# Performance work log

Hardware: AMD Instinct MI355X
Metric: run time of the kernel (lower is better)

## Reference

```python
import jax, jax.numpy as jnp
import numpy as np

C, H, W = 8, 2048, 2048
NUM_SEG = 64      # labels 0..63; label 0 = background (ndimage.label convention)
SIGMA_AGG = 0.5


def setup_inputs() -> dict:
    key = jax.random.key(0)
    k1, k2, k3 = jax.random.split(key, 3)
    pred_similarities = jax.random.normal(k1, (C, H, W), dtype=jnp.float32)
    kernel_labels = jax.random.randint(k2, (H, W), 0, NUM_SEG).astype(jnp.int32)
    region_labels = jax.random.randint(k3, (H, W), 0, NUM_SEG).astype(jnp.int32)
    # masks are 1 exactly where a connected component exists (labels > 0),
    # matching what ndimage.label would produce from these masks
    kernels_mask = (kernel_labels > 0).astype(jnp.float32)
    regions_mask = (region_labels > 0).astype(jnp.float32)
    return {
        "pred_similarities": pred_similarities,
        "regions_mask": regions_mask,
        "kernels_mask": kernels_mask,
        "kernel_labels": kernel_labels,
        "region_labels": region_labels,
    }


def reference(pred_similarities, regions_mask, kernels_mask, kernel_labels, region_labels):
    h, w = kernel_labels.shape
    kl = kernel_labels.reshape(-1)  # [N]
    rl = region_labels.reshape(-1)  # [N]

    # per-label cardinality, broadcast back to pixels (label 0 contributes 0
    # because the mask is 0 there, matching the original's untouched zeros)
    kcard = jax.ops.segment_sum(kernels_mask.reshape(-1), kl, num_segments=NUM_SEG)[kl].reshape(h, w)
    rcard = jax.ops.segment_sum(regions_mask.reshape(-1), rl, num_segments=NUM_SEG)[rl].reshape(h, w)

    # per-channel, per-kernel-component sum of pred, broadcast back per pixel
    c = pred_similarities.shape[0]
    pred_flat = pred_similarities.reshape(c, -1)  # [C, N]
    seg = jax.vmap(lambda p: jax.ops.segment_sum(p, kl, num_segments=NUM_SEG))(pred_flat)  # [C, NUM_SEG]
    Gk = jnp.where(kl[None, :] > 0, seg[:, kl], 0.0).reshape(c, h, w)
    Gk = Gk / (kcard + 1.0)[None]

    Fp = pred_similarities * regions_mask[None]
    diff = Fp - Gk
    # torch.linalg.norm over the whole tensor -> scalar Frobenius norm
    D = jnp.maximum(jnp.sqrt(jnp.sum(diff * diff)) - SIGMA_AGG, 0.0)
    per_pixel = jnp.log(D * D + 1.0) / (rcard + 1.0)  # [H, W]

    num_region = jnp.maximum(jnp.max(region_labels), 1).astype(per_pixel.dtype)
    return jnp.sum(per_pixel) / num_region
```

## Files before the change

kernel.cpp:

```cpp
#include <hip/hip_runtime.h>
#include <math.h>

#define NPIX (2048*2048)
#define NGROUPS (NPIX/32)
#define NBLOCKS 1024
#define NWAVES (NBLOCKS*4)

#define WS_FLOATS 3072
#define LROW 17
#define LTAB (64*LROW)
#define LDS_FLOATS (3*LTAB)

typedef __attribute__((ext_vector_type(8))) short short8;
typedef __attribute__((ext_vector_type(4))) float f32x4;
typedef __attribute__((ext_vector_type(2))) unsigned short u16x2;
typedef __attribute__((ext_vector_type(4))) unsigned int u32x4;

__device__ inline unsigned int pk_trunc_bf16(float lo, float hi) {
    return __builtin_amdgcn_perm(__float_as_uint(hi), __float_as_uint(lo), 0x07060302u);
}
__device__ inline unsigned int pk_lab(int lo, int hi) {
    return __builtin_amdgcn_perm((unsigned)hi, (unsigned)lo, 0x05040100u);
}
__device__ inline unsigned int onehot_pair(unsigned int x) {
    u16x2 xv = __builtin_bit_cast(u16x2, x);
    u16x2 y  = __builtin_elementwise_min(xv, (u16x2){1, 1});
    u16x2 w  = y - (u16x2){1, 1};
    return __builtin_bit_cast(unsigned int, w) & 0x3F803F80u;
}

__global__ __launch_bounds__(256, 4) void agg_mfma(
    const float* __restrict__ pred,
    const int*   __restrict__ kl,
    const int*   __restrict__ rl,
    float* __restrict__ ws)
{
    const int tid  = threadIdx.x;
    const int wv   = tid >> 6;
    const int lane = tid & 63;
    const int quad = lane >> 4;
    const int col  = lane & 15;
    const int c8   = col & 7;
    const bool lowcol = (col < 8);
    const unsigned int cpack   = (unsigned)col * 0x00010001u;
    const unsigned int hiconst = (col == 8) ? 0x3F803F80u : 0u;

    f32x4 acc[12];
    #pragma unroll
    for (int s = 0; s < 12; ++s) acc[s] = (f32x4){0.f, 0.f, 0.f, 0.f};

    const float* predc = pred + (size_t)c8 * NPIX;
    const int gw = blockIdx.x * 4 + wv;

    for (int g = gw; g < NGROUPS; g += NWAVES) {
        const int p8 = g * 32 + quad * 8;

        const int4 ka = *(const int4*)(kl + p8);
        const int4 kb = *(const int4*)(kl + p8 + 4);
        const int4 ra = *(const int4*)(rl + p8);
        const int4 rb = *(const int4*)(rl + p8 + 4);
        const float4 pa = *(const float4*)(predc + p8);
        const float4 pb = *(const float4*)(predc + p8 + 4);

        const int   klv[8] = {ka.x, ka.y, ka.z, ka.w, kb.x, kb.y, kb.z, kb.w};
        const int   rlv[8] = {ra.x, ra.y, ra.z, ra.w, rb.x, rb.y, rb.z, rb.w};
        const float pv[8]  = {pa.x, pa.y, pa.z, pa.w, pb.x, pb.y, pb.z, pb.w};

        float pr[8];
        #pragma unroll
        for (int j = 0; j < 8; ++j) pr[j] = (rlv[j] > 0) ? pv[j] : 0.f;

        unsigned int b1p[4], b2p[4], kp[4], rp[4];
        #pragma unroll
        for (int i = 0; i < 4; ++i) {
            const int j0 = 2 * i, j1 = 2 * i + 1;
            const float a0 = lowcol ? pv[j0] : pr[j0];
            const float a1 = lowcol ? pv[j1] : pr[j1];
            b1p[i] = pk_trunc_bf16(a0, a1);
            const unsigned int q = pk_trunc_bf16(pr[j0] * pr[j0], pr[j1] * pr[j1]);
            b2p[i] = lowcol ? q : hiconst;
            kp[i] = pk_lab(klv[j0], klv[j1]);
            rp[i] = pk_lab(rlv[j0], rlv[j1]);
        }
        const short8 b1 = __builtin_bit_cast(short8, (u32x4){b1p[0], b1p[1], b1p[2], b1p[3]});
        const short8 b2 = __builtin_bit_cast(short8, (u32x4){b2p[0], b2p[1], b2p[2], b2p[3]});

        #pragma unroll
        for (int t = 0; t < 4; ++t) {
            const unsigned int tp = cpack + (unsigned)t * 0x00100010u;
            u32x4 ohk, ohr;
            #pragma unroll
            for (int i = 0; i < 4; ++i) {
                ohk[i] = onehot_pair(kp[i] ^ tp);
                ohr[i] = onehot_pair(rp[i] ^ tp);
            }
            const short8 ak = __builtin_bit_cast(short8, ohk);
            const short8 ar = __builtin_bit_cast(short8, ohr);
            acc[t]     = __builtin_amdgcn_mfma_f32_16x16x32_bf16(ak, b1, acc[t],     0, 0, 0);
            acc[4 + t] = __builtin_amdgcn_mfma_f32_16x16x32_bf16(ak, b2, acc[4 + t], 0, 0, 0);
            acc[8 + t] = __builtin_amdgcn_mfma_f32_16x16x32_bf16(ar, b2, acc[8 + t], 0, 0, 0);
        }
    }

    __shared__ float sws[LDS_FLOATS];
    for (int w = 0; w < 4; ++w) {
        if (wv == w) {
            #pragma unroll
            for (int s = 0; s < 12; ++s) {
                const int T = s >> 2, t = s & 3;
                #pragma unroll
                for (int i = 0; i < 4; ++i) {
                    const int l = t * 16 + quad * 4 + i;
                    const int a = T * LTAB + l * LROW + col;
                    if (w == 0) sws[a] = acc[s][i];
                    else        sws[a] += acc[s][i];
                }
            }
        }
        __syncthreads();
    }
    for (int idx = tid; idx < WS_FLOATS; idx += 256) {
        const int T = idx >> 10, r = idx & 1023, l = r >> 4, c = r & 15;
        atomicAdd(&ws[idx], sws[T * LTAB + l * LROW + c]);
    }
}

__global__ __launch_bounds__(64) void agg_final(const float* __restrict__ ws,
                                                float* __restrict__ out)
{
    const int l = threadIdx.x;
    const float* t0 = ws + l * 16;
    const float* t1 = ws + 1024 + l * 16;
    const float* t2 = ws + 2048 + l * 16;

    float f2 = 0.f, corr = 0.f;
    #pragma unroll
    for (int c = 0; c < 8; ++c) f2 += t1[c];
    const float pck = t1[8];
    if (l > 0) {
        #pragma unroll
        for (int c = 0; c < 8; ++c) {
            const float gk = t0[c] / (pck + 1.f);
            corr += gk * (gk * pck - 2.f * t0[8 + c]);
        }
    }
    const float pcr   = t2[8];
    const float rcard = (l > 0) ? pcr : 0.f;
    float S = pcr / (rcard + 1.f);
    int mx = (pcr > 0.5f) ? l : 0;

    #pragma unroll
    for (int off = 32; off > 0; off >>= 1) {
        f2   += __shfl_down(f2, off, 64);
        corr += __shfl_down(corr, off, 64);
        S    += __shfl_down(S, off, 64);
        mx    = max(mx, __shfl_down(mx, off, 64));
    }
    if (l == 0) {
        const float SS = f2 + corr;
        float D = sqrtf(fmaxf(SS, 0.f)) - 0.5f;
        D = fmaxf(D, 0.f);
        out[0] = logf(D * D + 1.f) * S / (float)max(mx, 1);
    }
}

extern "C" void kernel_launch(void* const* d_in, const int* in_sizes, int n_in,
                              void* d_out, int out_size, void* d_ws, size_t ws_size,
                              hipStream_t stream) {
    const float* pred = (const float*)d_in[0];
    const int* kl = (const int*)d_in[3];
    const int* rl = (const int*)d_in[4];
    float* ws = (float*)d_ws;

    hipMemsetAsync(d_ws, 0, WS_FLOATS * sizeof(float), stream);
    agg_mfma<<<NBLOCKS, 256, 0, stream>>>(pred, kl, rl, ws);
    agg_final<<<1, 64, 0, stream>>>(ws, (float*)d_out);
}
```

Baseline: 264.6 us.

## Compute squared-norm in FP32 and simplify one-hot encoding for MFMA aggregation

```diff
diff --git a/kernel.cpp b/kernel.cpp
--- a/kernel.cpp
+++ b/kernel.cpp
@@ -3,17 +3,17 @@
 
 #define NPIX (2048*2048)
 #define NGROUPS (NPIX/32)
-#define NBLOCKS 1024
+#define NBLOCKS 1280
 #define NWAVES (NBLOCKS*4)
 
-#define WS_FLOATS 3072
+#define WS_FLOATS 3073
+#define WS_F2 3072
 #define LROW 17
 #define LTAB (64*LROW)
 #define LDS_FLOATS (3*LTAB)
 
 typedef __attribute__((ext_vector_type(8))) short short8;
 typedef __attribute__((ext_vector_type(4))) float f32x4;
-typedef __attribute__((ext_vector_type(2))) unsigned short u16x2;
 typedef __attribute__((ext_vector_type(4))) unsigned int u32x4;
 
 __device__ inline unsigned int pk_trunc_bf16(float lo, float hi) {
@@ -22,14 +22,13 @@
 __device__ inline unsigned int pk_lab(int lo, int hi) {
     return __builtin_amdgcn_perm((unsigned)hi, (unsigned)lo, 0x05040100u);
 }
-__device__ inline unsigned int onehot_pair(unsigned int x) {
-    u16x2 xv = __builtin_bit_cast(u16x2, x);
-    u16x2 y  = __builtin_elementwise_min(xv, (u16x2){1, 1});
-    u16x2 w  = y - (u16x2){1, 1};
-    return __builtin_bit_cast(unsigned int, w) & 0x3F803F80u;
+__device__ inline unsigned int onehot2(unsigned int x, unsigned int tp) {
+    const unsigned int a = x ^ tp;
+    const unsigned int t = 0x40004000u - a;
+    return t & 0x40004000u;
 }
 
-__global__ __launch_bounds__(256, 4) void agg_mfma(
+__global__ __launch_bounds__(256, 5) void agg_mfma(
     const float* __restrict__ pred,
     const int*   __restrict__ kl,
     const int*   __restrict__ rl,
@@ -42,12 +41,16 @@
     const int col  = lane & 15;
     const int c8   = col & 7;
     const bool lowcol = (col < 8);
-    const unsigned int cpack   = (unsigned)col * 0x00010001u;
-    const unsigned int hiconst = (col == 8) ? 0x3F803F80u : 0u;
+    const unsigned int cpack = (unsigned)col * 0x00010001u;
+    unsigned int tp0 = cpack, tp1 = cpack + 0x00100010u,
+                 tp2 = cpack + 0x00200020u, tp3 = cpack + 0x00300030u;
+    const unsigned int hc = (col == 8) ? 0x3F803F80u : 0u;
+    const short8 b2c = __builtin_bit_cast(short8, (u32x4){hc, hc, hc, hc});
 
     f32x4 acc[12];
     #pragma unroll
     for (int s = 0; s < 12; ++s) acc[s] = (f32x4){0.f, 0.f, 0.f, 0.f};
+    float f2 = 0.f;
 
     const float* predc = pred + (size_t)c8 * NPIX;
     const int gw = blockIdx.x * 4 + wv;
@@ -68,41 +71,47 @@
 
         float pr[8];
         #pragma unroll
-        for (int j = 0; j < 8; ++j) pr[j] = (rlv[j] > 0) ? pv[j] : 0.f;
+        for (int j = 0; j < 8; ++j) {
+            pr[j] = (rlv[j] > 0) ? pv[j] : 0.f;
+            f2 = fmaf(pr[j], pr[j], f2);
+        }
 
-        unsigned int b1p[4], b2p[4], kp[4], rp[4];
+        unsigned int b1p[4], kp[4], rp[4];
         #pragma unroll
         for (int i = 0; i < 4; ++i) {
             const int j0 = 2 * i, j1 = 2 * i + 1;
-            const float a0 = lowcol ? pv[j0] : pr[j0];
-            const float a1 = lowcol ? pv[j1] : pr[j1];
-            b1p[i] = pk_trunc_bf16(a0, a1);
-            const unsigned int q = pk_trunc_bf16(pr[j0] * pr[j0], pr[j1] * pr[j1]);
-            b2p[i] = lowcol ? q : hiconst;
-            kp[i] = pk_lab(klv[j0], klv[j1]);
-            rp[i] = pk_lab(rlv[j0], rlv[j1]);
+            const unsigned int plo = pk_trunc_bf16(pv[j0], pv[j1]);
+            const unsigned int phi = pk_trunc_bf16(pr[j0], pr[j1]);
+            b1p[i] = lowcol ? plo : phi;
+            kp[i]  = pk_lab(klv[j0], klv[j1]);
+            rp[i]  = pk_lab(rlv[j0], rlv[j1]);
         }
         const short8 b1 = __builtin_bit_cast(short8, (u32x4){b1p[0], b1p[1], b1p[2], b1p[3]});
-        const short8 b2 = __builtin_bit_cast(short8, (u32x4){b2p[0], b2p[1], b2p[2], b2p[3]});
 
+        const unsigned int tps[4] = {tp0, tp1, tp2, tp3};
         #pragma unroll
         for (int t = 0; t < 4; ++t) {
-            const unsigned int tp = cpack + (unsigned)t * 0x00100010u;
             u32x4 ohk, ohr;
             #pragma unroll
             for (int i = 0; i < 4; ++i) {
-                ohk[i] = onehot_pair(kp[i] ^ tp);
-                ohr[i] = onehot_pair(rp[i] ^ tp);
+                ohk[i] = onehot2(kp[i], tps[t]);
+                ohr[i] = onehot2(rp[i], tps[t]);
             }
             const short8 ak = __builtin_bit_cast(short8, ohk);
             const short8 ar = __builtin_bit_cast(short8, ohr);
-            acc[t]     = __builtin_amdgcn_mfma_f32_16x16x32_bf16(ak, b1, acc[t],     0, 0, 0);
-            acc[4 + t] = __builtin_amdgcn_mfma_f32_16x16x32_bf16(ak, b2, acc[4 + t], 0, 0, 0);
-            acc[8 + t] = __builtin_amdgcn_mfma_f32_16x16x32_bf16(ar, b2, acc[8 + t], 0, 0, 0);
+            acc[t]     = __builtin_amdgcn_mfma_f32_16x16x32_bf16(ak, b1,  acc[t],     0, 0, 0);
+            acc[4 + t] = __builtin_amdgcn_mfma_f32_16x16x32_bf16(ak, b2c, acc[4 + t], 0, 0, 0);
+            acc[8 + t] = __builtin_amdgcn_mfma_f32_16x16x32_bf16(ar, b2c, acc[8 + t], 0, 0, 0);
         }
     }
 
+    __shared__ float s_f2w[4];
+    #pragma unroll
+    for (int off = 32; off > 0; off >>= 1) f2 += __shfl_down(f2, off, 64);
+    if (lane == 0) s_f2w[wv] = f2;
+
     __shared__ float sws[LDS_FLOATS];
+    __syncthreads();
     for (int w = 0; w < 4; ++w) {
         if (wv == w) {
             #pragma unroll
@@ -119,7 +128,9 @@
         }
         __syncthreads();
     }
-    for (int idx = tid; idx < WS_FLOATS; idx += 256) {
+    if (tid == 0)
+        atomicAdd(&ws[WS_F2], s_f2w[0] + s_f2w[1] + s_f2w[2] + s_f2w[3]);
+    for (int idx = tid; idx < 3072; idx += 256) {
         const int T = idx >> 10, r = idx & 1023, l = r >> 4, c = r & 15;
         atomicAdd(&ws[idx], sws[T * LTAB + l * LROW + c]);
     }
@@ -133,21 +144,22 @@
     const float* t1 = ws + 1024 + l * 16;
     const float* t2 = ws + 2048 + l * 16;
 
-    float f2 = 0.f, corr = 0.f;
-    #pragma unroll
-    for (int c = 0; c < 8; ++c) f2 += t1[c];
-    const float pck = t1[8];
+    const float pck = 0.5f * t1[8];
+    const float pcr = 0.5f * t2[8];
+    float corr = 0.f;
     if (l > 0) {
         #pragma unroll
         for (int c = 0; c < 8; ++c) {
-            const float gk = t0[c] / (pck + 1.f);
-            corr += gk * (gk * pck - 2.f * t0[8 + c]);
+            const float seg = 0.5f * t0[c];
+            const float T   = 0.5f * t0[8 + c];
+            const float gk  = seg / (pck + 1.f);
+            corr += gk * (gk * pck - 2.f * T);
         }
     }
-    const float pcr   = t2[8];
     const float rcard = (l > 0) ? pcr : 0.f;
     float S = pcr / (rcard + 1.f);
     int mx = (pcr > 0.5f) ? l : 0;
+    float f2 = (l == 0) ? 0.5f * ws[WS_F2] : 0.f;
 
     #pragma unroll
     for (int off = 32; off > 0; off >>= 1) {
```

After: 263.0 us. Within noise of the previous version (-0.6%).
